# Performance work log

Hardware: AMD Instinct MI355X
Metric: run time of the kernel (lower is better)

Reference implementation:

```python
import jax, jax.numpy as jnp
import numpy as np

C_IN = 3072
C_OUT = 1024
MAJ = 3  # majority_size


def setup_inputs() -> dict:
    key = jax.random.key(0)
    k1, k2 = jax.random.split(key)
    x = jax.random.normal(k1, (256, C_IN), dtype=jnp.float32)
    stdv = 1.0 / np.sqrt(C_OUT * C_IN)
    weight = jax.random.uniform(k2, (C_OUT, C_IN), dtype=jnp.float32, minval=-stdv, maxval=stdv)
    return {"input": x, "weight": weight}


def reference(input, weight):
    B = input.shape[0]
    G = C_IN // MAJ  # number of majority groups
    # Deterministic binarization (sign), as in Binarize(..., 'det')
    xb = jnp.sign(input)            # [B, C_IN]
    wb = jnp.sign(weight)           # [C_OUT, C_IN]
    # Grouped products: inter[b,c,g] = sum_k xb[b,g,k] * wb[c,g,k]
    # (equivalent to einsum('bj,cj->bcj') followed by reshape+sum over groups of 3)
    xg = xb.reshape(B, G, MAJ)
    wg = wb.reshape(C_OUT, G, MAJ)
    inter = jnp.einsum('bgk,cgk->bcg', xg, wg)  # [B, C_OUT, G]
    # Majority vote: clamp group sums to [-1, 1], sum across groups, scale by 2.25
    out = jnp.sum(jnp.clip(inter, -1.0, 1.0), axis=2) * 2.25  # [B, C_OUT]
    return out
```

## Files before the change

kernel.cpp:

```cpp
#include <hip/hip_runtime.h>
#include <stdint.h>


#define C_IN  3072
#define C_OUT 1024


__global__ __launch_bounds__(256) void pack_x(const float* __restrict__ x,
                                              uint64_t* __restrict__ xpk) {
    int j    = blockIdx.x * 4 + (threadIdx.x >> 6);
    int lane = threadIdx.x & 63;
    int b = j >> 2, q = j & 3;
    const float4* s4 = (const float4*)(x + (size_t)b * C_IN + q * 768 + 12 * lane);
    float4 f0 = s4[0], f1 = s4[1], f2 = s4[2];
    float v[12] = {f0.x, f0.y, f0.z, f0.w,
                   f1.x, f1.y, f1.z, f1.w,
                   f2.x, f2.y, f2.z, f2.w};
    uint64_t pl[12];
#pragma unroll
    for (int m = 0; m < 12; ++m)
        pl[m] = __ballot(v[m] > 0.0f);
    if (lane == 0) {
        uint64_t* dst = xpk + ((size_t)b * 4 + q) * 12;
#pragma unroll
        for (int m = 0; m < 12; ++m)
            dst[m] = pl[m];
    }
}

__global__ __launch_bounds__(256) void fused_maj(const float* __restrict__ w,
                                                 const uint64_t* __restrict__ xpk,
                                                 float* __restrict__ out) {
    __shared__ uint64_t wpl[8][12];
    const int tid  = threadIdx.x;
    const int lane = tid & 63;
    const int wv   = tid >> 6;
    const int c0   = blockIdx.x * 2;

    for (int h = wv; h < 8; h += 4) {
        int cl = h >> 2, q = h & 3;
        const float4* s4 = (const float4*)(w + (size_t)(c0 + cl) * C_IN + q * 768 + 12 * lane);
        float4 f0 = s4[0], f1 = s4[1], f2 = s4[2];
        float v[12] = {f0.x, f0.y, f0.z, f0.w,
                       f1.x, f1.y, f1.z, f1.w,
                       f2.x, f2.y, f2.z, f2.w};
        uint64_t pl[12];
#pragma unroll
        for (int m = 0; m < 12; ++m)
            pl[m] = __ballot(v[m] > 0.0f);
        if (lane == 0) {
#pragma unroll
            for (int m = 0; m < 12; ++m)
                wpl[h][m] = pl[m];
        }
    }
    __syncthreads();

    const int b = tid;
    int acc0 = 0, acc1 = 0;
#pragma unroll
    for (int q = 0; q < 4; ++q) {
        const uint64_t* xb = xpk + ((size_t)b * 4 + q) * 12;
        uint64_t X[12];
#pragma unroll
        for (int m = 0; m < 12; ++m) X[m] = xb[m];
#pragma unroll
        for (int j = 0; j < 4; ++j) {
            uint64_t t0 = X[3 * j + 0] ^ wpl[q][3 * j + 0];
            uint64_t t1 = X[3 * j + 1] ^ wpl[q][3 * j + 1];
            uint64_t t2 = X[3 * j + 2] ^ wpl[q][3 * j + 2];
            acc0 += __popcll((t0 & t1) | (t2 & (t0 | t1)));
            uint64_t u0 = X[3 * j + 0] ^ wpl[4 + q][3 * j + 0];
            uint64_t u1 = X[3 * j + 1] ^ wpl[4 + q][3 * j + 1];
            uint64_t u2 = X[3 * j + 2] ^ wpl[4 + q][3 * j + 2];
            acc1 += __popcll((u0 & u1) | (u2 & (u0 | u1)));
        }
    }
    float2 r;
    r.x = 2304.0f - 4.5f * (float)acc0;
    r.y = 2304.0f - 4.5f * (float)acc1;
    *(float2*)(out + (size_t)b * C_OUT + c0) = r;
}

extern "C" void kernel_launch(void* const* d_in, const int* in_sizes, int n_in,
                              void* d_out, int out_size, void* d_ws, size_t ws_size,
                              hipStream_t stream) {
    const float* x = (const float*)d_in[0];
    const float* w = (const float*)d_in[1];
    float* out = (float*)d_out;

    uint64_t* xpk = (uint64_t*)d_ws;

    pack_x<<<256, 256, 0, stream>>>(x, xpk);
    fused_maj<<<512, 256, 0, stream>>>(w, xpk, out);
}
```

Baseline: 73.10 us.

## Fuse sign packing and majority popcount into one tiled kernel

Replaces the separate x-packing kernel and per-2-channel kernel with a single kernel where each block packs a 32-row x tile and a 32-row w tile into LDS, then each thread computes 4 output channels for one batch row. This removes a launch and the global packed-x intermediate and increases reuse of packed bits. In exchange, x and w rows are re-read and re-packed by many blocks, and each wave performs a long serial packing loop before any compute.

```diff
diff --git a/kernel.cpp b/kernel.cpp
--- a/kernel.cpp
+++ b/kernel.cpp
@@ -4,82 +4,85 @@
 
 #define C_IN  3072
 #define C_OUT 1024
+#define BT 32
+#define CT 32
+#define PSTR 49
 
+__global__ __launch_bounds__(256) void majfc_one(const float* __restrict__ x,
+                                                 const float* __restrict__ w,
+                                                 float* __restrict__ out) {
+    __shared__ uint64_t xp[BT][PSTR];
+    __shared__ uint64_t wp[CT][PSTR];
 
-__global__ __launch_bounds__(256) void pack_x(const float* __restrict__ x,
-                                              uint64_t* __restrict__ xpk) {
-    int j    = blockIdx.x * 4 + (threadIdx.x >> 6);
-    int lane = threadIdx.x & 63;
-    int b = j >> 2, q = j & 3;
-    const float4* s4 = (const float4*)(x + (size_t)b * C_IN + q * 768 + 12 * lane);
-    float4 f0 = s4[0], f1 = s4[1], f2 = s4[2];
-    float v[12] = {f0.x, f0.y, f0.z, f0.w,
-                   f1.x, f1.y, f1.z, f1.w,
-                   f2.x, f2.y, f2.z, f2.w};
-    uint64_t pl[12];
-#pragma unroll
-    for (int m = 0; m < 12; ++m)
-        pl[m] = __ballot(v[m] > 0.0f);
-    if (lane == 0) {
-        uint64_t* dst = xpk + ((size_t)b * 4 + q) * 12;
-#pragma unroll
-        for (int m = 0; m < 12; ++m)
-            dst[m] = pl[m];
-    }
-}
-
-__global__ __launch_bounds__(256) void fused_maj(const float* __restrict__ w,
-                                                 const uint64_t* __restrict__ xpk,
-                                                 float* __restrict__ out) {
-    __shared__ uint64_t wpl[8][12];
     const int tid  = threadIdx.x;
     const int lane = tid & 63;
     const int wv   = tid >> 6;
-    const int c0   = blockIdx.x * 2;
 
-    for (int h = wv; h < 8; h += 4) {
-        int cl = h >> 2, q = h & 3;
-        const float4* s4 = (const float4*)(w + (size_t)(c0 + cl) * C_IN + q * 768 + 12 * lane);
-        float4 f0 = s4[0], f1 = s4[1], f2 = s4[2];
-        float v[12] = {f0.x, f0.y, f0.z, f0.w,
-                       f1.x, f1.y, f1.z, f1.w,
-                       f2.x, f2.y, f2.z, f2.w};
-        uint64_t pl[12];
-#pragma unroll
-        for (int m = 0; m < 12; ++m)
-            pl[m] = __ballot(v[m] > 0.0f);
-        if (lane == 0) {
-#pragma unroll
-            for (int m = 0; m < 12; ++m)
-                wpl[h][m] = pl[m];
+    const int r  = blockIdx.x & 7;
+    const int s  = blockIdx.x >> 3;
+    const int ct = r * 4 + (s & 3);
+    const int bt = s >> 2;
+    const int b0 = bt * BT;
+    const int c0 = ct * CT;
+
+    {
+        const float* base = (wv & 2) ? (w + (size_t)c0 * C_IN) : (x + (size_t)b0 * C_IN);
+        uint64_t (*dst)[PSTR] = (wv & 2) ? wp : xp;
+        const int row0 = (wv & 1) * 16;
+#pragma unroll 4
+        for (int i = 0; i < 64; ++i) {
+            const int row = row0 + (i >> 2);
+            const int q   = i & 3;
+            const float4* s4 = (const float4*)(base + (size_t)row * C_IN + q * 768 + 12 * lane);
+            float4 f0 = s4[0], f1 = s4[1], f2 = s4[2];
+            uint64_t pl0  = __ballot(f0.x > 0.0f);
+            uint64_t pl1  = __ballot(f0.y > 0.0f);
+            uint64_t pl2  = __ballot(f0.z > 0.0f);
+            uint64_t pl3  = __ballot(f0.w > 0.0f);
+            uint64_t pl4  = __ballot(f1.x > 0.0f);
+            uint64_t pl5  = __ballot(f1.y > 0.0f);
+            uint64_t pl6  = __ballot(f1.z > 0.0f);
+            uint64_t pl7  = __ballot(f1.w > 0.0f);
+            uint64_t pl8  = __ballot(f2.x > 0.0f);
+            uint64_t pl9  = __ballot(f2.y > 0.0f);
+            uint64_t pl10 = __ballot(f2.z > 0.0f);
+            uint64_t pl11 = __ballot(f2.w > 0.0f);
+            if (lane == 0) {
+                uint64_t* d = &dst[row][q * 12];
+                d[0] = pl0;  d[1] = pl1;  d[2]  = pl2;  d[3]  = pl3;
+                d[4] = pl4;  d[5] = pl5;  d[6]  = pl6;  d[7]  = pl7;
+                d[8] = pl8;  d[9] = pl9;  d[10] = pl10; d[11] = pl11;
+            }
         }
     }
     __syncthreads();
 
-    const int b = tid;
-    int acc0 = 0, acc1 = 0;
+    const int bl = tid & 31;
+    const int cg = tid >> 5;
+    int acc[4] = {0, 0, 0, 0};
 #pragma unroll
     for (int q = 0; q < 4; ++q) {
-        const uint64_t* xb = xpk + ((size_t)b * 4 + q) * 12;
         uint64_t X[12];
 #pragma unroll
-        for (int m = 0; m < 12; ++m) X[m] = xb[m];
+        for (int m = 0; m < 12; ++m) X[m] = xp[bl][q * 12 + m];
 #pragma unroll
-        for (int j = 0; j < 4; ++j) {
-            uint64_t t0 = X[3 * j + 0] ^ wpl[q][3 * j + 0];
-            uint64_t t1 = X[3 * j + 1] ^ wpl[q][3 * j + 1];
-            uint64_t t2 = X[3 * j + 2] ^ wpl[q][3 * j + 2];
-            acc0 += __popcll((t0 & t1) | (t2 & (t0 | t1)));
-            uint64_t u0 = X[3 * j + 0] ^ wpl[4 + q][3 * j + 0];
-            uint64_t u1 = X[3 * j + 1] ^ wpl[4 + q][3 * j + 1];
-            uint64_t u2 = X[3 * j + 2] ^ wpl[4 + q][3 * j + 2];
-            acc1 += __popcll((u0 & u1) | (u2 & (u0 | u1)));
+        for (int jj = 0; jj < 4; ++jj) {
+            const uint64_t* W = &wp[cg * 4 + jj][q * 12];
+#pragma unroll
+            for (int j = 0; j < 4; ++j) {
+                uint64_t t0 = X[3 * j + 0] ^ W[3 * j + 0];
+                uint64_t t1 = X[3 * j + 1] ^ W[3 * j + 1];
+                uint64_t t2 = X[3 * j + 2] ^ W[3 * j + 2];
+                acc[jj] += __popcll((t0 & t1) | (t2 & (t0 | t1)));
+            }
         }
     }
-    float2 r;
-    r.x = 2304.0f - 4.5f * (float)acc0;
-    r.y = 2304.0f - 4.5f * (float)acc1;
-    *(float2*)(out + (size_t)b * C_OUT + c0) = r;
+    float4 res;
+    res.x = 2304.0f - 4.5f * (float)acc[0];
+    res.y = 2304.0f - 4.5f * (float)acc[1];
+    res.z = 2304.0f - 4.5f * (float)acc[2];
+    res.w = 2304.0f - 4.5f * (float)acc[3];
+    *(float4*)(out + (size_t)(b0 + bl) * C_OUT + c0 + cg * 4) = res;
 }
 
 extern "C" void kernel_launch(void* const* d_in, const int* in_sizes, int n_in,
@@ -88,9 +91,7 @@
     const float* x = (const float*)d_in[0];
     const float* w = (const float*)d_in[1];
     float* out = (float*)d_out;
+    (void)d_ws; (void)ws_size;
 
-    uint64_t* xpk = (uint64_t*)d_ws;
-
-    pack_x<<<256, 256, 0, stream>>>(x, xpk);
-    fused_maj<<<512, 256, 0, stream>>>(w, xpk, out);
+    majfc_one<<<256, 256, 0, stream>>>(x, w, out);
 }
```

After: 93.80 us. +28.3%, slower.
